# Optimization experiments

Hardware: AMD Instinct MI355X
Metric: run time of the kernel (lower is better)

Reference implementation:

```python
import jax, jax.numpy as jnp
import numpy as np

S, B, H = 256, 128, 512
V1, V2 = 30000, 64
E1, E2 = 128, 64
HOPS = 2
G = 3 * H  # gate dim (r,z,n)


def setup_inputs() -> dict:
    key = jax.random.key(0)
    ks = iter(jax.random.split(key, 48))
    def nrm(shape):
        return jax.random.normal(next(ks), shape, dtype=jnp.float32) * 0.05
    inp = {
        "input1_var": jax.random.randint(next(ks), (S, B), 0, V1),
        "input2_var": jax.random.randint(next(ks), (S, B), 0, V2),
        "input_length": jnp.full((B,), S, dtype=jnp.int32),  # full-length (packing is a no-op)
        "parse_graph": jax.random.randint(next(ks), (B, 3, S, S), 0, 2).astype(jnp.int32),
        "emb1": nrm((V1, E1)),
        "emb2": nrm((V2, E2)),
    }
    for l, d_in in ((0, E1 + E2), (1, 2 * H)):
        for d in ("f", "b"):
            inp[f"gru_wih{l}{d}"] = nrm((G, d_in))
            inp[f"gru_whh{l}{d}"] = nrm((G, H))
            inp[f"gru_bih{l}{d}"] = nrm((G,))
            inp[f"gru_bhh{l}{d}"] = nrm((G,))
    inp["gnn_fc1_w"] = nrm((HOPS, H, H)); inp["gnn_fc1_b"] = nrm((HOPS, H))
    inp["gnn_fc2_w"] = nrm((HOPS, H, H)); inp["gnn_fc2_b"] = nrm((HOPS, H))
    inp["gnn_out_w"] = nrm((HOPS, H, 2 * H)); inp["gnn_out_b"] = nrm((HOPS, H))
    return inp


def _gru_dir(x, W_ih, W_hh, b_ih, b_hh, reverse):
    # x: [S, B, d_in] -> (outputs [S, B, H], final hidden [B, H]); torch GRU equations
    xg = jnp.einsum('sbi,gi->sbg', x, W_ih) + b_ih  # precompute input gates [S,B,3H]
    h0 = jnp.zeros((x.shape[1], W_hh.shape[1] ), x.dtype)
    def step(h, xg_t):
        hg = h @ W_hh.T + b_hh
        xr, xz, xn = jnp.split(xg_t, 3, axis=-1)
        hr, hz, hn = jnp.split(hg, 3, axis=-1)
        r = jax.nn.sigmoid(xr + hr)
        z = jax.nn.sigmoid(xz + hz)
        n = jnp.tanh(xn + r * hn)
        h_new = (1.0 - z) * n + z * h
        return h_new, h_new
    hT, ys = jax.lax.scan(step, h0, xg, reverse=reverse)
    return ys, hT


def _forward(input1_var, input2_var, parse_graph, emb1, emb2, gru_params, gnn_fc1_w, gnn_fc1_b, gnn_fc2_w, gnn_fc2_b, gnn_out_w, gnn_out_b):
    emb2_eff = emb2.at[0].set(0.0)  # padding_idx=0
    x = jnp.concatenate([emb1[input1_var], emb2_eff[input2_var]], axis=-1)  # [S,B,E1+E2]
    # dropout: eval mode -> identity
    hiddens = []
    for (wih_f, whh_f, bih_f, bhh_f, wih_b, whh_b, bih_b, bhh_b) in gru_params:
        yf, hf = _gru_dir(x, wih_f, whh_f, bih_f, bhh_f, False)
        yb, hb = _gru_dir(x, wih_b, whh_b, bih_b, bhh_b, True)
        x = jnp.concatenate([yf, yb], axis=-1)  # [S,B,2H]
        hiddens += [hf, hb]
    pade_hidden = jnp.stack(hiddens, axis=0)  # [n_layers*2, B, H]
    out = x[..., :H] + x[..., H:]             # sum directions [S,B,H]
    node = jnp.swapaxes(out, 0, 1)            # [B,S,H]
    # GCN-style symmetric normalization with self-loops (same for every hop)
    A = parse_graph[:, 2].astype(node.dtype) + jnp.eye(S, dtype=node.dtype)
    dinv = 1.0 / jnp.sqrt(jnp.sum(A, axis=-1))
    An = A * dinv[:, :, None] * dinv[:, None, :]  # [B,S,S]
    for i in range(HOPS):
        ni = jax.nn.relu(jnp.einsum('bst,bth->bsh', An, node) @ gnn_fc1_w[i].T + gnn_fc1_b[i])
        ni = jax.nn.relu(jnp.einsum('bst,bth->bsh', An, ni) @ gnn_fc2_w[i].T + gnn_fc2_b[i])
        node = jax.nn.relu(jnp.concatenate([node, ni], axis=-1) @ gnn_out_w[i].T + gnn_out_b[i])
    pade_outputs = jnp.swapaxes(node, 0, 1)  # [S,B,H]
    return pade_outputs, pade_hidden


def reference(input1_var, input2_var, input_length, parse_graph, emb1, emb2,
              gru_wih0f, gru_whh0f, gru_bih0f, gru_bhh0f,
              gru_wih0b, gru_whh0b, gru_bih0b, gru_bhh0b,
              gru_wih1f, gru_whh1f, gru_bih1f, gru_bhh1f,
              gru_wih1b, gru_whh1b, gru_bih1b, gru_bhh1b,
              gnn_fc1_w, gnn_fc1_b, gnn_fc2_w, gnn_fc2_b, gnn_out_w, gnn_out_b):
    gru_params = [
        (gru_wih0f, gru_whh0f, gru_bih0f, gru_bhh0f, gru_wih0b, gru_whh0b, gru_bih0b, gru_bhh0b),
        (gru_wih1f, gru_whh1f, gru_bih1f, gru_bhh1f, gru_wih1b, gru_whh1b, gru_bih1b, gru_bhh1b),
    ]
    return _forward(input1_var, input2_var, parse_graph, emb1, emb2, gru_params,
                    gnn_fc1_w, gnn_fc1_b, gnn_fc2_w, gnn_fc2_b, gnn_out_w, gnn_out_b)
```

## Files before the change

kernel.cpp:

```cpp
#include <hip/hip_runtime.h>
#include <hip/hip_bf16.h>

using short8 = __attribute__((ext_vector_type(8))) short;
using f32x4  = __attribute__((ext_vector_type(4))) float;
typedef unsigned short u16;
typedef unsigned int u32;

#define S_LEN 256
#define BATCH 128
#define HID   512
#define GATE  1536
#define SB    32768

static __device__ __forceinline__ u16 f2b(float f){
  union { float f; u32 u; } v; v.f = f;
  u32 r = v.u + 0x7fffu + ((v.u >> 16) & 1u);
  return (u16)(r >> 16);
}
static __device__ __forceinline__ float b2f(u16 h){
  union { u32 u; float f; } v; v.u = ((u32)h) << 16; return v.f;
}
static __device__ __forceinline__ f32x4 mfma16(short8 a, short8 b, f32x4 c){
  return __builtin_amdgcn_mfma_f32_16x16x32_bf16(a, b, c, 0, 0, 0);
}

static __device__ __forceinline__ void load16_coherent(uint4* dst, const void* p){
  asm volatile("global_load_dwordx4 %0, %1, off sc0 sc1"
               : "=v"(*dst) : "v"(p) : "memory");
}
static __device__ __forceinline__ void store4_coherent(void* p, u32 v){
  asm volatile("global_store_dword %0, %1, off sc0 sc1"
               :: "v"(p), "v"(v) : "memory");
}
static __device__ __forceinline__ void wait_vm0(){
  asm volatile("s_waitcnt vmcnt(0)" ::: "memory");
}


__global__ void fill_zero(float* p, long n){
  long i = (long)blockIdx.x * blockDim.x + threadIdx.x;
  long st = (long)gridDim.x * blockDim.x;
  for (; i < n; i += st) p[i] = 0.f;
}

__global__ void cvt_bf16(const float* in, u16* out, long n){
  long i = (long)blockIdx.x * blockDim.x + threadIdx.x;
  long st = (long)gridDim.x * blockDim.x;
  for (; i < n; i += st) out[i] = f2b(in[i]);
}

__global__ void permute_rows(const float* in, u16* out, int K){
  long n = (long)GATE * K;
  long i = (long)blockIdx.x * blockDim.x + threadIdx.x;
  long st = (long)gridDim.x * blockDim.x;
  for (; i < n; i += st){
    int orow = (int)(i / K); int k = (int)(i - (long)orow * K);
    int g = orow >> 9, c = orow & 511;
    int nrow = ((c >> 4) * 48) + (g << 4) + (c & 15);
    out[(long)nrow * K + k] = f2b(in[i]);
  }
}

__global__ void permute_bias(const float* in, float* out){
  int orow = blockIdx.x * blockDim.x + threadIdx.x;
  if (orow < GATE){
    int g = orow >> 9, c = orow & 511;
    out[((c >> 4) * 48) + (g << 4) + (c & 15)] = in[orow];
  }
}

__global__ void embed_kernel(const int* __restrict__ i1, const int* __restrict__ i2,
                             const float* __restrict__ e1, const float* __restrict__ e2,
                             u16* __restrict__ x0){
  int row = blockIdx.x; int t = threadIdx.x;
  float v;
  if (t < 128) v = e1[(long)i1[row] * 128 + t];
  else { int ix = i2[row]; v = ix ? e2[(long)ix * 64 + (t - 128)] : 0.f; }
  x0[(long)row * 192 + t] = f2b(v);
}

__global__ __launch_bounds__(256) void gemm_bt(
    const u16* __restrict__ A, int lda, long sAz,
    const u16* __restrict__ W, int ldw, long sWz,
    const float* __restrict__ bias,
    u16* __restrict__ Cb, int ldc, long sCz,
    float* __restrict__ Cf,
    int K, int flags)
{
  __shared__ u16 As[128 * 40];
  __shared__ u16 Ws[128 * 40];
  const int tid = threadIdx.x;
  const int m0 = blockIdx.x * 128, n0 = blockIdx.y * 128;
  const long z = blockIdx.z;
  const u16* Ab = A + z * sAz;
  const u16* Wb = W + z * sWz;
  const int r0 = tid >> 2, kg = (tid & 3) * 8;
  const int lane = tid & 63, w = tid >> 6;
  const int wr = w >> 1, wc = w & 1;
  const int col = lane & 15, q = lane >> 4;
  f32x4 acc[4][4];
#pragma unroll
  for (int i = 0; i < 4; i++)
#pragma unroll
    for (int j = 0; j < 4; j++) acc[i][j] = (f32x4){0.f, 0.f, 0.f, 0.f};

  for (int k0 = 0; k0 < K; k0 += 32){
    uint4 a0 = *(const uint4*)(Ab + (long)(m0 + r0) * lda + k0 + kg);
    uint4 a1 = *(const uint4*)(Ab + (long)(m0 + r0 + 64) * lda + k0 + kg);
    uint4 w0 = *(const uint4*)(Wb + (long)(n0 + r0) * ldw + k0 + kg);
    uint4 w1 = *(const uint4*)(Wb + (long)(n0 + r0 + 64) * ldw + k0 + kg);
    __syncthreads();
    *(uint4*)(As + r0 * 40 + kg) = a0;
    *(uint4*)(As + (r0 + 64) * 40 + kg) = a1;
    *(uint4*)(Ws + r0 * 40 + kg) = w0;
    *(uint4*)(Ws + (r0 + 64) * 40 + kg) = w1;
    __syncthreads();
    short8 af[4], bf[4];
#pragma unroll
    for (int i = 0; i < 4; i++) af[i] = *(const short8*)(As + (wr * 64 + i * 16 + col) * 40 + q * 8);
#pragma unroll
    for (int j = 0; j < 4; j++) bf[j] = *(const short8*)(Ws + (wc * 64 + j * 16 + col) * 40 + q * 8);
#pragma unroll
    for (int i = 0; i < 4; i++)
#pragma unroll
      for (int j = 0; j < 4; j++)
        acc[i][j] = mfma16(af[i], bf[j], acc[i][j]);
  }

#pragma unroll
  for (int i = 0; i < 4; i++)
#pragma unroll
    for (int j = 0; j < 4; j++){
      int n = n0 + wc * 64 + j * 16 + col;
      float bv = bias ? bias[n] : 0.f;
#pragma unroll
      for (int r = 0; r < 4; r++){
        int m = m0 + wr * 64 + i * 16 + q * 4 + r;
        float v = acc[i][j][r] + bv;
        if (flags & 1) v = fmaxf(v, 0.f);
        if (Cb) Cb[z * sCz + (long)m * ldc + n] = f2b(v);
        if (Cf){ int s = m & 255, b = m >> 8; Cf[((long)s * 128 + b) * 512 + n] = v; }
      }
    }
}

__global__ __launch_bounds__(64) void gru_persist(
    const u16* __restrict__ whh,
    const float* __restrict__ bhh,
    const u16* __restrict__ xg,
    u16* __restrict__ hbf,
    u16* __restrict__ y_cat,
    u16* __restrict__ y_node,
    float* __restrict__ hT,
    u32* __restrict__ flags)
{
  const int bid = blockIdx.x;
  const int dir = bid >> 7, r7 = bid & 127;
  const int cb = r7 >> 3, bt = r7 & 7, b0 = bt * 16;
  const int lane = threadIdx.x, col = lane & 15, q = lane >> 4;
  u32* gflag = flags + (dir * 8 + bt) * 16;
  u32* myflag = gflag + cb;

  __shared__ u16 Ws[96 * 520];
  {
    const u16* Wd = whh + (long)dir * GATE * HID + (long)(96 * cb) * HID;
    for (int i = lane; i < 96 * 64; i += 64){
      int row = i >> 6, k8 = (i & 63) << 3;
      *(short8*)(Ws + row * 520 + k8) = *(const short8*)(Wd + (long)row * HID + k8);
    }
  }
  __syncthreads();

  const u16* xgd = xg + (long)dir * SB * GATE;
  const float* bh = bhh + dir * GATE;
  float bhv[2][3];
#pragma unroll
  for (int cg = 0; cg < 2; cg++)
#pragma unroll
    for (int g = 0; g < 3; g++)
      bhv[cg][g] = bh[48 * (2 * cb + cg) + 16 * g + col];

  float hold[2][4];
#pragma unroll
  for (int cg = 0; cg < 2; cg++)
#pragma unroll
    for (int r = 0; r < 4; r++) hold[cg][r] = 0.f;

  for (int s = 0; s < 256; s++){
    const int t = dir ? (255 - s) : s;
    u16 xv[2][4][3];
#pragma unroll
    for (int cg = 0; cg < 2; cg++)
#pragma unroll
      for (int r = 0; r < 4; r++){
        const u16* xp = xgd + ((long)t * BATCH + (b0 + q * 4 + r)) * GATE + 48 * (2 * cb + cg);
#pragma unroll
        for (int g = 0; g < 3; g++) xv[cg][r][g] = xp[16 * g + col];
      }
    if (s){
      const u32 tgt = (u32)s;
      for (;;){
        u32 v = __hip_atomic_load(gflag + (lane & 15), __ATOMIC_RELAXED, __HIP_MEMORY_SCOPE_AGENT);
        if (__ballot(v >= tgt) == ~0ull) break;
        __builtin_amdgcn_s_sleep(1);
      }
    }
    const u16* hin = hbf + ((long)((s & 1) * 2 + dir)) * (BATCH * HID);
    u16* hout = hbf + ((long)(((s & 1) ^ 1) * 2 + dir)) * (BATCH * HID);

    uint4 hreg[16];
#pragma unroll
    for (int kk = 0; kk < 16; kk++)
      load16_coherent(&hreg[kk], hin + (long)(b0 + col) * HID + kk * 32 + q * 8);
    wait_vm0();

    f32x4 acc[6];
#pragma unroll
    for (int tl = 0; tl < 6; tl++) acc[tl] = (f32x4){0.f, 0.f, 0.f, 0.f};

#pragma unroll
    for (int kk = 0; kk < 16; kk++){
      short8 a8 = *(const short8*)&hreg[kk];
#pragma unroll
      for (int tl = 0; tl < 6; tl++){
        short8 bfr = *(const short8*)(Ws + (tl * 16 + col) * 520 + kk * 32 + q * 8);
        acc[tl] = mfma16(a8, bfr, acc[tl]);
      }
    }

#pragma unroll
    for (int cg = 0; cg < 2; cg++)
#pragma unroll
      for (int r = 0; r < 4; r++){
        int b = b0 + q * 4 + r;
        int c = cb * 32 + cg * 16 + col;
        float xr = b2f(xv[cg][r][0]);
        float xz = b2f(xv[cg][r][1]);
        float xn = b2f(xv[cg][r][2]);
        float gr = 1.f / (1.f + expf(-(xr + acc[cg * 3 + 0][r] + bhv[cg][0])));
        float gz = 1.f / (1.f + expf(-(xz + acc[cg * 3 + 1][r] + bhv[cg][1])));
        float gn = tanhf(xn + gr * (acc[cg * 3 + 2][r] + bhv[cg][2]));
        float hnew = (1.f - gz) * gn + gz * hold[cg][r];
        hold[cg][r] = hnew;
        u16 hb = f2b(hnew);
        if (y_cat)  y_cat[((long)t * BATCH + b) * 1024 + dir * HID + c] = hb;
        if (y_node) y_node[((long)b * 256 + t) * 1024 + dir * HID + c] = hb;
        u32 mine = (u32)hb;
        u32 other = (u32)__shfl_xor((int)mine, 1);
        if (!(lane & 1))
          store4_coherent(hout + (long)b * HID + c, mine | (other << 16));
      }
    wait_vm0();
    if (lane == 0) atomicAdd(myflag, 1u);
  }

#pragma unroll
  for (int cg = 0; cg < 2; cg++)
#pragma unroll
    for (int r = 0; r < 4; r++){
      int b = b0 + q * 4 + r;
      int c = cb * 32 + cg * 16 + col;
      hT[(long)dir * BATCH * HID + (long)b * HID + c] = hold[cg][r];
    }
}

__global__ void combine_cat(u16* __restrict__ cat){
  long n = (long)SB * HID;
  long i = (long)blockIdx.x * blockDim.x + threadIdx.x;
  long st = (long)gridDim.x * blockDim.x;
  for (; i < n; i += st){
    long row = i >> 9; int c = (int)(i & 511);
    u16* p = cat + row * 1024;
    p[c] = f2b(b2f(p[c]) + b2f(p[512 + c]));
  }
}


__global__ __launch_bounds__(64) void deg_kernel(const int* __restrict__ pg, float* __restrict__ dinv){
  int i = blockIdx.x, b = blockIdx.y, lane = threadIdx.x;
  const int* p = pg + ((long)b * 3 + 2) * 65536 + i * 256 + lane * 4;
  int4 v = *(const int4*)p;
  int s = v.x + v.y + v.z + v.w;
  for (int o = 32; o; o >>= 1) s += __shfl_down(s, o);
  if (lane == 0) dinv[b * 256 + i] = 1.f / sqrtf((float)(s + 1));
}

__global__ void an_kernel(const int* __restrict__ pg, const float* __restrict__ dinv, u16* __restrict__ An){
  int j = threadIdx.x, i = blockIdx.x, b = blockIdx.y;
  float a = (float)pg[((long)b * 3 + 2) * 65536 + i * 256 + j] + (i == j ? 1.f : 0.f);
  An[((long)b * 256 + i) * 256 + j] = f2b(a * dinv[b * 256 + i] * dinv[b * 256 + j]);
}

__global__ void transpose_bf16(const u16* __restrict__ in, long sIn, int ldin,
                               u16* __restrict__ out, long sOut, int R){
  __shared__ u16 tile[32][33];
  const u16* ip = in + (long)blockIdx.z * sIn;
  u16* op = out + (long)blockIdx.z * sOut;
  int r0 = blockIdx.x * 32, c0 = blockIdx.y * 32;
  for (int yy = threadIdx.y; yy < 32; yy += 8)
    tile[yy][threadIdx.x] = ip[(long)(r0 + yy) * ldin + c0 + threadIdx.x];
  __syncthreads();
  for (int yy = threadIdx.y; yy < 32; yy += 8)
    op[(long)(c0 + yy) * R + r0 + threadIdx.x] = tile[threadIdx.x][yy];
}


extern "C" void kernel_launch(void* const* d_in, const int* in_sizes, int n_in,
                              void* d_out, int out_size, void* d_ws, size_t ws_size,
                              hipStream_t stream)
{
  const int* i1 = (const int*)d_in[0];
  const int* i2 = (const int*)d_in[1];
  const int* pg = (const int*)d_in[3];
  const float* e1 = (const float*)d_in[4];
  const float* e2 = (const float*)d_in[5];
  const float* wih[2][2]  = {{(const float*)d_in[6],  (const float*)d_in[10]},
                             {(const float*)d_in[14], (const float*)d_in[18]}};
  const float* whhI[2][2] = {{(const float*)d_in[7],  (const float*)d_in[11]},
                             {(const float*)d_in[15], (const float*)d_in[19]}};
  const float* bihI[2][2] = {{(const float*)d_in[8],  (const float*)d_in[12]},
                             {(const float*)d_in[16], (const float*)d_in[20]}};
  const float* bhhI[2][2] = {{(const float*)d_in[9],  (const float*)d_in[13]},
                             {(const float*)d_in[17], (const float*)d_in[21]}};
  const float* fc1w = (const float*)d_in[22]; const float* fc1b = (const float*)d_in[23];
  const float* fc2w = (const float*)d_in[24]; const float* fc2b = (const float*)d_in[25];
  const float* outw = (const float*)d_in[26]; const float* outb = (const float*)d_in[27];
  float* out = (float*)d_out;

  char* wp = (char*)d_ws;
  auto alloc = [&](size_t bytes) -> void* {
    void* r = (void*)wp; wp += (bytes + 255) & ~(size_t)255; return r;
  };
  const int dins[2] = {192, 1024};

  char* ubase = wp;
  u16* xg = (u16*)alloc((size_t)2 * SB * GATE * 2);
  u16* An    = (u16*)(ubase);
  u16* nodeT = (u16*)(ubase + 16777216);
  u16* t1    = (u16*)(ubase + 50331648);
  u16* nib   = (u16*)(ubase + 83886080);
  u16* cat1  = (u16*)(ubase + 117440512);

  u16* x1b  = (u16*)alloc((size_t)SB * 1024 * 2);
  u16* cat0 = x1b;

  u16* x0b   = (u16*)alloc((size_t)SB * 192 * 2);
  u16* hbf   = (u16*)alloc((size_t)2 * 2 * BATCH * HID * 2);
  u32* ctr   = (u32*)alloc((size_t)16 * 16 * 4);
  float* dinv= (float*)alloc((size_t)BATCH * S_LEN * 4);
  u16* wihp[2][2]; u16* whhp[2][2]; float* bihp[2][2]; float* bhhp[2][2];
  for (int l = 0; l < 2; l++)
    for (int d = 0; d < 2; d++) wihp[l][d] = (u16*)alloc((size_t)GATE * dins[l] * 2);
  for (int l = 0; l < 2; l++)
    for (int d = 0; d < 2; d++) whhp[l][d] = (u16*)alloc((size_t)GATE * HID * 2);
  for (int l = 0; l < 2; l++)
    for (int d = 0; d < 2; d++) bihp[l][d] = (float*)alloc((size_t)GATE * 4);
  for (int l = 0; l < 2; l++)
    for (int d = 0; d < 2; d++) bhhp[l][d] = (float*)alloc((size_t)GATE * 4);
  u16* fc1wb = (u16*)alloc((size_t)2 * HID * HID * 2);
  u16* fc2wb = (u16*)alloc((size_t)2 * HID * HID * 2);
  u16* outwb = (u16*)alloc((size_t)2 * HID * 1024 * 2);

  size_t need = (size_t)(wp - (char*)d_ws);
  if (need > ws_size) return;

  for (int l = 0; l < 2; l++)
    for (int d = 0; d < 2; d++){
      permute_rows<<<256, 256, 0, stream>>>(wih[l][d], wihp[l][d], dins[l]);
      permute_rows<<<256, 256, 0, stream>>>(whhI[l][d], whhp[l][d], HID);
      permute_bias<<<6, 256, 0, stream>>>(bihI[l][d], bihp[l][d]);
      permute_bias<<<6, 256, 0, stream>>>(bhhI[l][d], bhhp[l][d]);
    }
  cvt_bf16<<<512, 256, 0, stream>>>(fc1w, fc1wb, (long)2 * HID * HID);
  cvt_bf16<<<512, 256, 0, stream>>>(fc2w, fc2wb, (long)2 * HID * HID);
  cvt_bf16<<<512, 256, 0, stream>>>(outw, outwb, (long)2 * HID * 1024);
  embed_kernel<<<SB, 192, 0, stream>>>(i1, i2, e1, e2, x0b);

  auto gemm = [&](const u16* A, int lda, long sAz, const u16* W, int ldw, long sWz,
                  const float* bias, u16* Cb, int ldc, long sCz, float* Cf,
                  int M, int N, int K, int Z, int flags){
    dim3 g(M / 128, N / 128, Z);
    gemm_bt<<<g, 256, 0, stream>>>(A, lda, sAz, W, ldw, sWz, bias, Cb, ldc, sCz, Cf, K, flags);
  };

  for (int l = 0; l < 2; l++){
    const u16* xin = l ? x1b : x0b; int K = dins[l];
    for (int d = 0; d < 2; d++)
      gemm(xin, K, 0, wihp[l][d], K, 0, bihp[l][d],
           xg + (long)d * SB * GATE, GATE, 0, nullptr, SB, GATE, K, 1, 0);
    fill_zero<<<128, 256, 0, stream>>>((float*)hbf, (long)(2 * 2 * BATCH * HID) / 2);
    fill_zero<<<1, 256, 0, stream>>>((float*)ctr, 256);
    const u16* whh_l = whhp[l][0];
    const float* bhh_l = bhhp[l][0];
    u16* ycat = (l == 0) ? x1b : nullptr;
    u16* ynode = (l == 0) ? nullptr : cat0;
    float* hT = out + (long)SB * HID + (long)l * 2 * BATCH * HID;
    void* args[8] = { (void*)&whh_l, (void*)&bhh_l, (void*)&xg, (void*)&hbf,
                      (void*)&ycat, (void*)&ynode, (void*)&hT, (void*)&ctr };
    hipError_t e = hipLaunchCooperativeKernel((const void*)gru_persist, dim3(256), dim3(64),
                                              args, 0, stream);
    (void)e;
  }

  combine_cat<<<2048, 256, 0, stream>>>(cat0);
  deg_kernel<<<dim3(256, 128), 64, 0, stream>>>(pg, dinv);
  an_kernel<<<dim3(256, 128), 256, 0, stream>>>(pg, dinv, An);

  u16* cc = cat0; u16* cn = cat1;
  for (int hop = 0; hop < 2; hop++){
    transpose_bf16<<<dim3(8, 16, 128), dim3(32, 8), 0, stream>>>(
        cc, (long)S_LEN * 1024, 1024, nodeT, (long)HID * S_LEN, S_LEN);
    gemm(An, 256, (long)S_LEN * S_LEN, nodeT, 256, (long)HID * S_LEN, nullptr,
         t1, HID, (long)S_LEN * HID, nullptr, S_LEN, HID, S_LEN, BATCH, 0);
    gemm(t1, HID, 0, fc1wb + (long)hop * HID * HID, HID, 0, fc1b + hop * HID,
         nib, HID, 0, nullptr, SB, HID, HID, 1, 1);
    transpose_bf16<<<dim3(8, 16, 128), dim3(32, 8), 0, stream>>>(
        nib, (long)S_LEN * HID, HID, nodeT, (long)HID * S_LEN, S_LEN);
    gemm(An, 256, (long)S_LEN * S_LEN, nodeT, 256, (long)HID * S_LEN, nullptr,
         t1, HID, (long)S_LEN * HID, nullptr, S_LEN, HID, S_LEN, BATCH, 0);
    gemm(t1, HID, 0, fc2wb + (long)hop * HID * HID, HID, 0, fc2b + hop * HID,
         cc + HID, 1024, 0, nullptr, SB, HID, HID, 1, 1);
    gemm(cc, 1024, 0, outwb + (long)hop * HID * 1024, 1024, 0, outb + hop * HID,
         (hop == 1) ? nullptr : cn, 1024, 0, (hop == 1) ? out : nullptr, SB, HID, 1024, 1, 1);
    u16* tmp = cc; cc = cn; cn = tmp;
  }
}
```

Baseline: 4.154 ms.

## Interleave both GRU directions within each persistent block to hide barrier latency

Each persistent block now owns a 16-column slice for both the forward and backward direction, rather than a 32-column slice of a single direction. It alternates between the two directions every step, so the wait on one direction's flag barrier overlaps with the other direction's matvec. Per-direction flag groups grow to 32 blocks, and the y_cat/y_node stores move after the flag increment, off the critical path. The trade-off is that each barrier now waits on twice as many peer blocks, and each step runs smaller MFMA batches (3 tiles instead of 6) per barrier.

```diff
diff --git a/kernel.cpp b/kernel.cpp
--- a/kernel.cpp
+++ b/kernel.cpp
@@ -155,112 +155,116 @@
     u32* __restrict__ flags)
 {
   const int bid = blockIdx.x;
-  const int dir = bid >> 7, r7 = bid & 127;
-  const int cb = r7 >> 3, bt = r7 & 7, b0 = bt * 16;
+  const int cs = bid >> 3, bt = bid & 7, b0 = bt * 16;
   const int lane = threadIdx.x, col = lane & 15, q = lane >> 4;
-  u32* gflag = flags + (dir * 8 + bt) * 16;
-  u32* myflag = gflag + cb;
-
-  __shared__ u16 Ws[96 * 520];
-  {
-    const u16* Wd = whh + (long)dir * GATE * HID + (long)(96 * cb) * HID;
-    for (int i = lane; i < 96 * 64; i += 64){
+  const int c = cs * 16 + col;
+
+  __shared__ u16 Ws[2][48 * 520];
+#pragma unroll
+  for (int d = 0; d < 2; d++){
+    const u16* Wd = whh + (long)d * GATE * HID + (long)(48 * cs) * HID;
+    for (int i = lane; i < 48 * 64; i += 64){
       int row = i >> 6, k8 = (i & 63) << 3;
-      *(short8*)(Ws + row * 520 + k8) = *(const short8*)(Wd + (long)row * HID + k8);
+      *(short8*)(&Ws[d][0] + row * 520 + k8) = *(const short8*)(Wd + (long)row * HID + k8);
     }
   }
   __syncthreads();
 
-  const u16* xgd = xg + (long)dir * SB * GATE;
-  const float* bh = bhh + dir * GATE;
   float bhv[2][3];
 #pragma unroll
-  for (int cg = 0; cg < 2; cg++)
+  for (int d = 0; d < 2; d++)
 #pragma unroll
     for (int g = 0; g < 3; g++)
-      bhv[cg][g] = bh[48 * (2 * cb + cg) + 16 * g + col];
+      bhv[d][g] = bhh[d * GATE + 48 * cs + 16 * g + col];
 
   float hold[2][4];
 #pragma unroll
-  for (int cg = 0; cg < 2; cg++)
-#pragma unroll
-    for (int r = 0; r < 4; r++) hold[cg][r] = 0.f;
+  for (int d = 0; d < 2; d++)
+#pragma unroll
+    for (int r = 0; r < 4; r++) hold[d][r] = 0.f;
 
   for (int s = 0; s < 256; s++){
-    const int t = dir ? (255 - s) : s;
     u16 xv[2][4][3];
 #pragma unroll
-    for (int cg = 0; cg < 2; cg++)
+    for (int d = 0; d < 2; d++){
+      const int t = d ? (255 - s) : s;
+      const u16* xgd = xg + (long)d * SB * GATE + 48 * cs;
 #pragma unroll
       for (int r = 0; r < 4; r++){
-        const u16* xp = xgd + ((long)t * BATCH + (b0 + q * 4 + r)) * GATE + 48 * (2 * cb + cg);
-#pragma unroll
-        for (int g = 0; g < 3; g++) xv[cg][r][g] = xp[16 * g + col];
-      }
-    if (s){
-      const u32 tgt = (u32)s;
-      for (;;){
-        u32 v = __hip_atomic_load(gflag + (lane & 15), __ATOMIC_RELAXED, __HIP_MEMORY_SCOPE_AGENT);
-        if (__ballot(v >= tgt) == ~0ull) break;
-        __builtin_amdgcn_s_sleep(1);
-      }
-    }
-    const u16* hin = hbf + ((long)((s & 1) * 2 + dir)) * (BATCH * HID);
-    u16* hout = hbf + ((long)(((s & 1) ^ 1) * 2 + dir)) * (BATCH * HID);
-
-    uint4 hreg[16];
-#pragma unroll
-    for (int kk = 0; kk < 16; kk++)
-      load16_coherent(&hreg[kk], hin + (long)(b0 + col) * HID + kk * 32 + q * 8);
-    wait_vm0();
-
-    f32x4 acc[6];
-#pragma unroll
-    for (int tl = 0; tl < 6; tl++) acc[tl] = (f32x4){0.f, 0.f, 0.f, 0.f};
-
-#pragma unroll
-    for (int kk = 0; kk < 16; kk++){
-      short8 a8 = *(const short8*)&hreg[kk];
-#pragma unroll
-      for (int tl = 0; tl < 6; tl++){
-        short8 bfr = *(const short8*)(Ws + (tl * 16 + col) * 520 + kk * 32 + q * 8);
-        acc[tl] = mfma16(a8, bfr, acc[tl]);
-      }
-    }
-
-#pragma unroll
-    for (int cg = 0; cg < 2; cg++)
+        const u16* xp = xgd + ((long)t * BATCH + (b0 + q * 4 + r)) * GATE;
+#pragma unroll
+        for (int g = 0; g < 3; g++) xv[d][r][g] = xp[16 * g + col];
+      }
+    }
+
+#pragma unroll
+    for (int d = 0; d < 2; d++){
+      const int t = d ? (255 - s) : s;
+      u32* gf = flags + (d * 8 + bt) * 32;
+      if (s){
+        const u32 tgt = (u32)s;
+        for (;;){
+          u32 v = __hip_atomic_load(gf + (lane & 31), __ATOMIC_RELAXED, __HIP_MEMORY_SCOPE_AGENT);
+          if (__ballot(v >= tgt) == ~0ull) break;
+          __builtin_amdgcn_s_sleep(1);
+        }
+      }
+      const u16* hin = hbf + ((long)((s & 1) * 2 + d)) * (BATCH * HID);
+      u16* hout = hbf + ((long)(((s & 1) ^ 1) * 2 + d)) * (BATCH * HID);
+
+      uint4 hreg[16];
+#pragma unroll
+      for (int kk = 0; kk < 16; kk++)
+        load16_coherent(&hreg[kk], hin + (long)(b0 + col) * HID + kk * 32 + q * 8);
+      wait_vm0();
+
+      f32x4 acc[3];
+#pragma unroll
+      for (int g = 0; g < 3; g++) acc[g] = (f32x4){0.f, 0.f, 0.f, 0.f};
+#pragma unroll
+      for (int kk = 0; kk < 16; kk++){
+        short8 a8 = *(const short8*)&hreg[kk];
+#pragma unroll
+        for (int g = 0; g < 3; g++){
+          short8 bfr = *(const short8*)(&Ws[d][0] + (16 * g + col) * 520 + kk * 32 + q * 8);
+          acc[g] = mfma16(a8, bfr, acc[g]);
+        }
+      }
+
+      u16 hbs[4];
+#pragma unroll
+      for (int r = 0; r < 4; r++){
+        float xr = b2f(xv[d][r][0]);
+        float xz = b2f(xv[d][r][1]);
+        float xn = b2f(xv[d][r][2]);
+        float gr = 1.f / (1.f + expf(-(xr + acc[0][r] + bhv[d][0])));
+        float gz = 1.f / (1.f + expf(-(xz + acc[1][r] + bhv[d][1])));
+        float gn = tanhf(xn + gr * (acc[2][r] + bhv[d][2]));
+        float hnew = (1.f - gz) * gn + gz * hold[d][r];
+        hold[d][r] = hnew;
+        hbs[r] = f2b(hnew);
+        u32 mine = (u32)hbs[r];
+        u32 other = (u32)__shfl_xor((int)mine, 1);
+        if (!(lane & 1))
+          store4_coherent(hout + (long)(b0 + q * 4 + r) * HID + c, mine | (other << 16));
+      }
+      wait_vm0();
+      if (lane == 0) atomicAdd(gf + cs, 1u);
 #pragma unroll
       for (int r = 0; r < 4; r++){
         int b = b0 + q * 4 + r;
-        int c = cb * 32 + cg * 16 + col;
-        float xr = b2f(xv[cg][r][0]);
-        float xz = b2f(xv[cg][r][1]);
-        float xn = b2f(xv[cg][r][2]);
-        float gr = 1.f / (1.f + expf(-(xr + acc[cg * 3 + 0][r] + bhv[cg][0])));
-        float gz = 1.f / (1.f + expf(-(xz + acc[cg * 3 + 1][r] + bhv[cg][1])));
-        float gn = tanhf(xn + gr * (acc[cg * 3 + 2][r] + bhv[cg][2]));
-        float hnew = (1.f - gz) * gn + gz * hold[cg][r];
-        hold[cg][r] = hnew;
-        u16 hb = f2b(hnew);
-        if (y_cat)  y_cat[((long)t * BATCH + b) * 1024 + dir * HID + c] = hb;
-        if (y_node) y_node[((long)b * 256 + t) * 1024 + dir * HID + c] = hb;
-        u32 mine = (u32)hb;
-        u32 other = (u32)__shfl_xor((int)mine, 1);
-        if (!(lane & 1))
-          store4_coherent(hout + (long)b * HID + c, mine | (other << 16));
-      }
-    wait_vm0();
-    if (lane == 0) atomicAdd(myflag, 1u);
-  }
-
-#pragma unroll
-  for (int cg = 0; cg < 2; cg++)
+        if (y_cat)  y_cat[((long)t * BATCH + b) * 1024 + d * HID + c] = hbs[r];
+        if (y_node) y_node[((long)b * 256 + t) * 1024 + d * HID + c] = hbs[r];
+      }
+    }
+  }
+
+#pragma unroll
+  for (int d = 0; d < 2; d++)
 #pragma unroll
     for (int r = 0; r < 4; r++){
       int b = b0 + q * 4 + r;
-      int c = cb * 32 + cg * 16 + col;
-      hT[(long)dir * BATCH * HID + (long)b * HID + c] = hold[cg][r];
+      hT[(long)d * BATCH * HID + (long)b * HID + c] = hold[d][r];
     }
 }
 
@@ -346,7 +350,7 @@
 
   u16* x0b   = (u16*)alloc((size_t)SB * 192 * 2);
   u16* hbf   = (u16*)alloc((size_t)2 * 2 * BATCH * HID * 2);
-  u32* ctr   = (u32*)alloc((size_t)16 * 16 * 4);
+  u32* ctr   = (u32*)alloc((size_t)2 * 8 * 32 * 4);
   float* dinv= (float*)alloc((size_t)BATCH * S_LEN * 4);
   u16* wihp[2][2]; u16* whhp[2][2]; float* bihp[2][2]; float* bhhp[2][2];
   for (int l = 0; l < 2; l++)
@@ -389,7 +393,7 @@
       gemm(xin, K, 0, wihp[l][d], K, 0, bihp[l][d],
            xg + (long)d * SB * GATE, GATE, 0, nullptr, SB, GATE, K, 1, 0);
     fill_zero<<<128, 256, 0, stream>>>((float*)hbf, (long)(2 * 2 * BATCH * HID) / 2);
-    fill_zero<<<1, 256, 0, stream>>>((float*)ctr, 256);
+    fill_zero<<<1, 256, 0, stream>>>((float*)ctr, 512);
     const u16* whh_l = whhp[l][0];
     const float* bhh_l = bhhp[l][0];
     u16* ycat = (l == 0) ? x1b : nullptr;
```

New measurement: 4.771 ms. 1.15x slower.
